# Performance work log

Hardware: AMD Instinct MI355X
Metric: run time of the kernel (lower is better)

The kernel has to match this reference:

```python
import jax, jax.numpy as jnp
import numpy as np

WIN = 9  # window_size (isotropic, module default)
EPS = 1e-5


def _box_sum3d(x, win):
    """Sum over a win^3 box, same-size output ('same' padding). x: [B,1,D,H,W].
    The ones kernel is separable, so apply three 1D convolutions."""
    pad = win // 2
    for ax in range(3):  # spatial axes D,H,W
        kshape = [1, 1, 1, 1, 1]
        kshape[2 + ax] = win
        k = jnp.ones(kshape, x.dtype)
        padding = [(0, 0)] * 3
        padding[ax] = (pad, pad)
        x = jax.lax.conv_general_dilated(x, k, window_strides=(1, 1, 1), padding=padding)
    return x


def setup_inputs() -> dict:
    key = jax.random.key(0)
    k1, k2 = jax.random.split(key)
    shape = (2, 1, 160, 192, 160)
    y_pred = jax.random.normal(k1, shape, dtype=jnp.float32)
    y_true = jax.random.normal(k2, shape, dtype=jnp.float32)
    return {"y_pred": y_pred, "y_true": y_true}


def reference(y_pred, y_true):
    I, J = y_true, y_pred
    win_size = jnp.asarray(WIN ** 3, I.dtype)  # 729

    I_sum = _box_sum3d(I, WIN)
    J_sum = _box_sum3d(J, WIN)
    I2_sum = _box_sum3d(I * I, WIN)
    J2_sum = _box_sum3d(J * J, WIN)
    IJ_sum = _box_sum3d(I * J, WIN)

    I_mean = I_sum / win_size
    J_mean = J_sum / win_size

    cross = IJ_sum - J_mean * I_sum - I_mean * J_sum + I_mean * J_mean * win_size
    I_var = I2_sum - 2 * I_mean * I_sum + I_mean * I_mean * win_size
    J_var = J2_sum - 2 * J_mean * J_sum + J_mean * J_mean * win_size

    cc = cross * cross / (I_var * J_var + EPS)
    return -jnp.mean(cc)
```

## Files before the change

kernel.cpp:

```cpp
#include <hip/hip_runtime.h>
#include <hip/hip_fp16.h>


#define B_    2
#define D_    160
#define H_    192
#define W_    160
#define HW_   (H_*W_)

#define RS    20
#define SLS   (24*RS)
#define FS    (2*SLS)
#define ZROW  4800
#define TMP0  4816
#define TS    20
#define HSUM0 (TMP0 + 4*320)
#define HCS   160
#define HRS   10
#define REDU  (HSUM0 + 10*HCS)
#define SMEM  (REDU + 8)
#define DC    40
#define NMAC  24
#define W3I   (1.0f/729.0f)
#define NTOT  9830400.0f

#if __has_builtin(__builtin_amdgcn_rcpf)
#define RCP(x) __builtin_amdgcn_rcpf(x)
#else
#define RCP(x) (1.0f/(x))
#endif
#define LGKM0() asm volatile("s_waitcnt lgkmcnt(0)" ::: "memory")

typedef _Float16 half8 __attribute__((ext_vector_type(8)));
typedef float    f32x4 __attribute__((ext_vector_type(4)));
#define MFMA16(a,b,c) __builtin_amdgcn_mfma_f32_16x16x32_f16((a),(b),(c),0,0,0)

struct __align__(8) HP { __half2 a, b; };

__global__ __launch_bounds__(256, 4) void ncc_fused(const float* __restrict__ gI,
                                                    const float* __restrict__ gJ,
                                                    float* __restrict__ out)
{
  __shared__ __align__(16) float sm[SMEM];
  const int tid  = threadIdx.x;
  const int lane = tid & 63;
  const int Q    = tid >> 6;
  const int n15  = lane & 15;
  const int q4   = lane >> 4;
  const int w0   = blockIdx.x * 16;
  const int h0   = blockIdx.y * 16;
  const int bz   = blockIdx.z;
  const int bb   = bz >> 2;
  const int d_lo = (bz & 3) * DC;

  for (int i = tid; i < TMP0; i += 256) sm[i] = 0.f;

  half8 SEL;
  #pragma unroll
  for (int j = 0; j < 8; ++j) {
    const int k = 8*q4 + j;
    SEL[j] = (k >= n15 && k <= n15 + 8) ? (_Float16)1 : (_Float16)0;
  }

  bool val0 = false, val1 = false;
  int  lo0 = 0, lo1 = 0, sc0 = 0, sc1 = 0;
  const float *pi0 = gI, *pj0 = gJ, *pi1 = gI, *pj1 = gJ;
  {
    auto prep = [&](int t, bool& val, int& lo, int& sc,
                    const float*& pi, const float*& pj) {
      if (t >= 288) { val = false; return; }
      sc = t / 144;
      const int u = t - sc*144;
      const int r = u / 6, c = u - r*6;
      const int gh = h0 - 4 + r, gw = w0 - 4 + 4*c;
      val = ((unsigned)gh < (unsigned)H_) && (gw >= 0) && (gw + 3 < W_);
      lo  = sc*SLS + r*RS + 2*c;
      const long off = ((long)(bb*D_ + (d_lo - 4 + sc))*H_ + gh)*(long)W_ + gw;
      pi = gI + off; pj = gJ + off;
    };
    prep(tid, val0, lo0, sc0, pi0, pj0);
    prep((tid >= 224) ? tid + 32 : 512, val1, lo1, sc1, pi1, pj1);
  }

  int rb_[3], hb_[3];
  #pragma unroll
  for (int i = 0; i < 3; ++i) {
    int c = Q + 4*i; if (c > 9) c = 9;
    rb_[i] = (c % 5)*FS + (c / 5)*SLS;
    hb_[i] = HSUM0 + c*HCS;
  }
  const int tb  = TMP0 + Q*320 + n15*TS;
  const int a1r = n15*RS + 4*q4;
  const int a2r = (n15 < 8) ? ((16 + n15)*RS + 4*q4) : -1;
  const int zr  = ZROW + 4*q4;

  const int rh = tid >> 4, rw = tid & 15;
  const int rbase = HSUM0 + rw*HRS + (rh >> 1);
  const int rsh   = (rh & 1) * 16;

  float ring[5][9], S[5];
  #pragma unroll
  for (int f = 0; f < 5; ++f) {
    S[f] = 0.f;
    #pragma unroll
    for (int k = 0; k < 9; ++k) ring[f][k] = 0.f;
  }
  float acc = 0.f;

  float4 f0i = {0,0,0,0}, f0j = {0,0,0,0}, f1i = {0,0,0,0}, f1j = {0,0,0,0};
  auto fetch = [&](int sbase) {
    if (val0 && (unsigned)(sbase + sc0) < (unsigned)D_) {
      f0i = *(const float4*)pi0; f0j = *(const float4*)pj0;
    } else { f0i = make_float4(0,0,0,0); f0j = make_float4(0,0,0,0); }
    pi0 += 2*HW_; pj0 += 2*HW_;
    if (val1 && (unsigned)(sbase + sc1) < (unsigned)D_) {
      f1i = *(const float4*)pi1; f1j = *(const float4*)pj1;
    } else { f1i = make_float4(0,0,0,0); f1j = make_float4(0,0,0,0); }
    pi1 += 2*HW_; pj1 += 2*HW_;
  };

  auto stage_one = [&](int lo, float4 fi, float4 fj) {
    const __half2 i01 = __floats2half2_rn(fi.x, fi.y);
    const __half2 i23 = __floats2half2_rn(fi.z, fi.w);
    const __half2 j01 = __floats2half2_rn(fj.x, fj.y);
    const __half2 j23 = __floats2half2_rn(fj.z, fj.w);
    HP hI; hI.a = i01; hI.b = i23;
    HP hJ; hJ.a = j01; hJ.b = j23;
    HP h2; h2.a = __hmul2(i01, i01); h2.b = __hmul2(i23, i23);
    HP h3; h3.a = __hmul2(j01, j01); h3.b = __hmul2(j23, j23);
    HP h4; h4.a = __hmul2(i01, j01); h4.b = __hmul2(i23, j23);
    *(HP*)&sm[lo]        = hI;
    *(HP*)&sm[lo +   FS] = hJ;
    *(HP*)&sm[lo + 2*FS] = h2;
    *(HP*)&sm[lo + 3*FS] = h3;
    *(HP*)&sm[lo + 4*FS] = h4;
  };
  auto stage_write = [&]() {
    if (val0) stage_one(lo0, f0i, f0j);
    if (val1) stage_one(lo1, f1i, f1j);
  };

  auto chain = [&](int rb, int hb) {
    const half8 A1 = *(const half8*)&sm[rb + a1r];
    const half8 A2 = (a2r >= 0) ? *(const half8*)&sm[rb + a2r]
                                : *(const half8*)&sm[zr];
    const f32x4 z = {0.f, 0.f, 0.f, 0.f};
    const f32x4 d1 = MFMA16(A1, SEL, z);
    const f32x4 d2 = MFMA16(A2, SEL, z);
    HP p1; p1.a = __floats2half2_rn(d1[0], d1[1]); p1.b = __floats2half2_rn(d1[2], d1[3]);
    HP p2; p2.a = __floats2half2_rn(d2[0], d2[1]); p2.b = __floats2half2_rn(d2[2], d2[3]);
    *(HP*)&sm[tb + 2*q4]     = p1;
    *(HP*)&sm[tb + 8 + 2*q4] = p2;
    LGKM0();
    const half8 Bh = *(const half8*)&sm[tb + 4*q4];
    const f32x4 dh = MFMA16(SEL, Bh, z);
    HP ph; ph.a = __floats2half2_rn(dh[0], dh[1]); ph.b = __floats2half2_rn(dh[2], dh[3]);
    *(HP*)&sm[hb + n15*HRS + 2*q4] = ph;
  };

  auto h2ext = [&](int addr) -> float {
    const unsigned u = *(const unsigned*)&sm[addr];
    return __half2float(__ushort_as_half((unsigned short)(u >> rsh)));
  };
  auto ring_cc = [&](int m) {
    float nA[5], nB[5];
    #pragma unroll
    for (int f = 0; f < 5; ++f) {
      nA[f] = h2ext(rbase + f*HCS);
      nB[f] = h2ext(rbase + (5 + f)*HCS);
    }
    float SA[5], SB[5];
    #pragma unroll
    for (int f = 0; f < 5; ++f) {
      SA[f] = S[f]  + nA[f] - ring[f][8];
      SB[f] = SA[f] + nB[f] - ring[f][7];
      S[f]  = SB[f];
      #pragma unroll
      for (int k = 8; k >= 2; --k) ring[f][k] = ring[f][k-2];
      ring[f][1] = nA[f]; ring[f][0] = nB[f];
    }
    if (m >= 4) {
      {
        const float cr = SA[4] - SA[0]*SA[1]*W3I;
        const float vi = SA[2] - SA[0]*SA[0]*W3I;
        const float vj = SA[3] - SA[1]*SA[1]*W3I;
        acc += cr*cr * RCP(vi*vj + 1e-5f);
      }
      {
        const float cr = SB[4] - SB[0]*SB[1]*W3I;
        const float vi = SB[2] - SB[0]*SB[0]*W3I;
        const float vj = SB[3] - SB[1]*SB[1]*W3I;
        acc += cr*cr * RCP(vi*vj + 1e-5f);
      }
    }
  };

  fetch(d_lo - 4);
  __syncthreads();
  stage_write();
  fetch(d_lo - 2);
  __syncthreads();

  for (int m = 0; m < NMAC; ++m) {
    chain(rb_[0], hb_[0]);
    chain(rb_[1], hb_[1]);
    if (Q < 2) chain(rb_[2], hb_[2]);
    __syncthreads();
    ring_cc(m);
    if (m + 1 < NMAC) { stage_write(); fetch(d_lo + 2*m); }
    __syncthreads();
  }

  float v = acc;
  #pragma unroll
  for (int off = 32; off > 0; off >>= 1)
    v += __shfl_down(v, off, 64);
  if (lane == 0) sm[REDU + Q] = v;
  __syncthreads();
  if (tid == 0) {
    const float t = sm[REDU] + sm[REDU+1] + sm[REDU+2] + sm[REDU+3];
    atomicAdd(out, -t / NTOT);
  }
}

extern "C" void kernel_launch(void* const* d_in, const int* in_sizes, int n_in,
                              void* d_out, int out_size, void* d_ws, size_t ws_size,
                              hipStream_t stream) {
  const float* J = (const float*)d_in[0];
  const float* I = (const float*)d_in[1];
  float* outp = (float*)d_out;
  hipMemsetAsync(d_out, 0, sizeof(float), stream);
  dim3 grid(W_/16, H_/16, B_*4);
  ncc_fused<<<grid, dim3(256), 0, stream>>>(I, J, outp);
}
```

Before: 147.5 us.

## Widen per-thread staging loads to 8 columns and pad slices to 32 rows

```diff
diff --git a/kernel.cpp b/kernel.cpp
--- a/kernel.cpp
+++ b/kernel.cpp
@@ -9,10 +9,9 @@
 #define HW_   (H_*W_)
 
 #define RS    20
-#define SLS   (24*RS)
+#define SLS   (32*RS)
 #define FS    (2*SLS)
-#define ZROW  4800
-#define TMP0  4816
+#define TMP0  (5*FS)
 #define TS    20
 #define HSUM0 (TMP0 + 4*320)
 #define HCS   160
@@ -35,7 +34,8 @@
 typedef float    f32x4 __attribute__((ext_vector_type(4)));
 #define MFMA16(a,b,c) __builtin_amdgcn_mfma_f32_16x16x32_f16((a),(b),(c),0,0,0)
 
-struct __align__(8) HP { __half2 a, b; };
+struct __align__(8)  HP  { __half2 a, b; };
+struct __align__(16) HP4 { __half2 a, b, c, d; };
 
 __global__ __launch_bounds__(256, 4) void ncc_fused(const float* __restrict__ gI,
                                                     const float* __restrict__ gJ,
@@ -62,37 +62,31 @@
     SEL[j] = (k >= n15 && k <= n15 + 8) ? (_Float16)1 : (_Float16)0;
   }
 
-  bool val0 = false, val1 = false;
-  int  lo0 = 0, lo1 = 0, sc0 = 0, sc1 = 0;
-  const float *pi0 = gI, *pj0 = gJ, *pi1 = gI, *pj1 = gJ;
-  {
-    auto prep = [&](int t, bool& val, int& lo, int& sc,
-                    const float*& pi, const float*& pj) {
-      if (t >= 288) { val = false; return; }
-      sc = t / 144;
-      const int u = t - sc*144;
-      const int r = u / 6, c = u - r*6;
-      const int gh = h0 - 4 + r, gw = w0 - 4 + 4*c;
-      val = ((unsigned)gh < (unsigned)H_) && (gw >= 0) && (gw + 3 < W_);
-      lo  = sc*SLS + r*RS + 2*c;
-      const long off = ((long)(bb*D_ + (d_lo - 4 + sc))*H_ + gh)*(long)W_ + gw;
-      pi = gI + off; pj = gJ + off;
-    };
-    prep(tid, val0, lo0, sc0, pi0, pj0);
-    prep((tid >= 224) ? tid + 32 : 512, val1, lo1, sc1, pi1, pj1);
-  }
-
-  int rb_[3], hb_[3];
-  #pragma unroll
-  for (int i = 0; i < 3; ++i) {
-    int c = Q + 4*i; if (c > 9) c = 9;
-    rb_[i] = (c % 5)*FS + (c / 5)*SLS;
-    hb_[i] = HSUM0 + c*HCS;
-  }
+  const bool tval = (tid < 144);
+  bool rowv = false, hv0 = false, hv1 = false;
+  int  lo = 0, sc = 0;
+  const float *pI = gI, *pJ = gJ;
+  if (tval) {
+    sc = tid / 72;
+    const int u = tid - sc*72;
+    const int r = u / 3, ci = u - 3*r;
+    const int gh = h0 - 4 + r;
+    const int gw = w0 - 4 + 8*ci;
+    rowv = (unsigned)gh < (unsigned)H_;
+    hv0  = rowv && ((unsigned)gw < (unsigned)(W_-3));
+    hv1  = rowv && ((unsigned)(gw+4) < (unsigned)(W_-3));
+    lo   = sc*SLS + r*RS + 4*ci;
+    const long off = ((long)(bb*D_ + (d_lo - 4 + sc))*H_ + gh)*(long)W_ + gw;
+    pI = gI + off; pJ = gJ + off;
+  }
+
+  auto rb_of = [&](int c) { return (c % 5)*FS + (c / 5)*SLS; };
+  const int cA = Q, cB = Q + 4, cC = Q + 6;
+  const int rbA = rb_of(cA), rbB = rb_of(cB), rbC = rb_of(cC);
+  const int hbA = HSUM0 + cA*HCS, hbB = HSUM0 + cB*HCS, hbC = HSUM0 + cC*HCS;
   const int tb  = TMP0 + Q*320 + n15*TS;
   const int a1r = n15*RS + 4*q4;
-  const int a2r = (n15 < 8) ? ((16 + n15)*RS + 4*q4) : -1;
-  const int zr  = ZROW + 4*q4;
+  const int a2r = (16 + n15)*RS + 4*q4;
 
   const int rh = tid >> 4, rw = tid & 15;
   const int rbase = HSUM0 + rw*HRS + (rh >> 1);
@@ -107,43 +101,45 @@
   }
   float acc = 0.f;
 
-  float4 f0i = {0,0,0,0}, f0j = {0,0,0,0}, f1i = {0,0,0,0}, f1j = {0,0,0,0};
+  float4 ai0 = {0,0,0,0}, ai1 = {0,0,0,0}, aj0 = {0,0,0,0}, aj1 = {0,0,0,0};
   auto fetch = [&](int sbase) {
-    if (val0 && (unsigned)(sbase + sc0) < (unsigned)D_) {
-      f0i = *(const float4*)pi0; f0j = *(const float4*)pj0;
-    } else { f0i = make_float4(0,0,0,0); f0j = make_float4(0,0,0,0); }
-    pi0 += 2*HW_; pj0 += 2*HW_;
-    if (val1 && (unsigned)(sbase + sc1) < (unsigned)D_) {
-      f1i = *(const float4*)pi1; f1j = *(const float4*)pj1;
-    } else { f1i = make_float4(0,0,0,0); f1j = make_float4(0,0,0,0); }
-    pi1 += 2*HW_; pj1 += 2*HW_;
-  };
-
-  auto stage_one = [&](int lo, float4 fi, float4 fj) {
-    const __half2 i01 = __floats2half2_rn(fi.x, fi.y);
-    const __half2 i23 = __floats2half2_rn(fi.z, fi.w);
-    const __half2 j01 = __floats2half2_rn(fj.x, fj.y);
-    const __half2 j23 = __floats2half2_rn(fj.z, fj.w);
-    HP hI; hI.a = i01; hI.b = i23;
-    HP hJ; hJ.a = j01; hJ.b = j23;
-    HP h2; h2.a = __hmul2(i01, i01); h2.b = __hmul2(i23, i23);
-    HP h3; h3.a = __hmul2(j01, j01); h3.b = __hmul2(j23, j23);
-    HP h4; h4.a = __hmul2(i01, j01); h4.b = __hmul2(i23, j23);
-    *(HP*)&sm[lo]        = hI;
-    *(HP*)&sm[lo +   FS] = hJ;
-    *(HP*)&sm[lo + 2*FS] = h2;
-    *(HP*)&sm[lo + 3*FS] = h3;
-    *(HP*)&sm[lo + 4*FS] = h4;
-  };
+    const bool dv = tval && ((unsigned)(sbase + sc) < (unsigned)D_);
+    const bool v0 = dv && hv0, v1 = dv && hv1;
+    ai0 = v0 ? *(const float4*)pI       : make_float4(0,0,0,0);
+    ai1 = v1 ? *(const float4*)(pI + 4) : make_float4(0,0,0,0);
+    aj0 = v0 ? *(const float4*)pJ       : make_float4(0,0,0,0);
+    aj1 = v1 ? *(const float4*)(pJ + 4) : make_float4(0,0,0,0);
+    pI += 2*HW_; pJ += 2*HW_;
+  };
+
   auto stage_write = [&]() {
-    if (val0) stage_one(lo0, f0i, f0j);
-    if (val1) stage_one(lo1, f1i, f1j);
+    if (!(tval && rowv)) return;
+    const __half2 iA = __floats2half2_rn(ai0.x, ai0.y);
+    const __half2 iB = __floats2half2_rn(ai0.z, ai0.w);
+    const __half2 iC = __floats2half2_rn(ai1.x, ai1.y);
+    const __half2 iD = __floats2half2_rn(ai1.z, ai1.w);
+    const __half2 jA = __floats2half2_rn(aj0.x, aj0.y);
+    const __half2 jB = __floats2half2_rn(aj0.z, aj0.w);
+    const __half2 jC = __floats2half2_rn(aj1.x, aj1.y);
+    const __half2 jD = __floats2half2_rn(aj1.z, aj1.w);
+    HP4 hI; hI.a = iA; hI.b = iB; hI.c = iC; hI.d = iD;
+    HP4 hJ; hJ.a = jA; hJ.b = jB; hJ.c = jC; hJ.d = jD;
+    HP4 h2; h2.a = __hmul2(iA,iA); h2.b = __hmul2(iB,iB);
+            h2.c = __hmul2(iC,iC); h2.d = __hmul2(iD,iD);
+    HP4 h3; h3.a = __hmul2(jA,jA); h3.b = __hmul2(jB,jB);
+            h3.c = __hmul2(jC,jC); h3.d = __hmul2(jD,jD);
+    HP4 h4; h4.a = __hmul2(iA,jA); h4.b = __hmul2(iB,jB);
+            h4.c = __hmul2(iC,jC); h4.d = __hmul2(iD,jD);
+    *(HP4*)&sm[lo]        = hI;
+    *(HP4*)&sm[lo +   FS] = hJ;
+    *(HP4*)&sm[lo + 2*FS] = h2;
+    *(HP4*)&sm[lo + 3*FS] = h3;
+    *(HP4*)&sm[lo + 4*FS] = h4;
   };
 
   auto chain = [&](int rb, int hb) {
     const half8 A1 = *(const half8*)&sm[rb + a1r];
-    const half8 A2 = (a2r >= 0) ? *(const half8*)&sm[rb + a2r]
-                                : *(const half8*)&sm[zr];
+    const half8 A2 = *(const half8*)&sm[rb + a2r];
     const f32x4 z = {0.f, 0.f, 0.f, 0.f};
     const f32x4 d1 = MFMA16(A1, SEL, z);
     const f32x4 d2 = MFMA16(A2, SEL, z);
@@ -202,9 +198,9 @@
   __syncthreads();
 
   for (int m = 0; m < NMAC; ++m) {
-    chain(rb_[0], hb_[0]);
-    chain(rb_[1], hb_[1]);
-    if (Q < 2) chain(rb_[2], hb_[2]);
+    chain(rbA, hbA);
+    chain(rbB, hbB);
+    if (Q >= 2) chain(rbC, hbC);
     __syncthreads();
     ring_cc(m);
     if (m + 1 < NMAC) { stage_write(); fetch(d_lo + 2*m); }
```

New measurement: 148.2 us. About the same (+0.4%).
